# Performance work log

Hardware: AMD Instinct MI355X
Metric: run time of the kernel (lower is better)

Reference implementation:

```python
import jax, jax.numpy as jnp
import numpy as np
from math import tan, cos, sin

FOVX, FOVY = 1.2, 0.9
ZNEAR, ZFAR = 0.1, 100.0
HEIGHT, WIDTH = 1080, 1920
RELAX = 1.3
N = 2_000_000


def get_projection_matrix():
    # faithful to Camera.get_projection_matrix (symmetric frustum)
    right = ZNEAR * tan(0.5 * FOVX)
    top = ZNEAR * tan(0.5 * FOVY)
    left, bottom = -right, -top
    return jnp.array([
        [2 * ZNEAR / (right - left), 0.0, (left + right) / (right - left), 0.0],
        [0.0, 2 * ZNEAR / (top - bottom), (top + bottom) / (top - bottom), 0.0],
        [0.0, 0.0, ZFAR / (ZFAR - ZNEAR), -ZFAR * ZNEAR / (ZFAR - ZNEAR)],
        [0.0, 0.0, 1.0, 0.0]], dtype=jnp.float32)


def setup_inputs() -> dict:
    key = jax.random.key(0)
    k1, k2, k3 = jax.random.split(key, 3)
    # Gaussians spread in front of the camera: xy ~ N(0,3^2), z in [0.5, 20]
    xy = 3.0 * jax.random.normal(k1, (N, 2), dtype=jnp.float32)
    z = jax.random.uniform(k2, (N, 1), dtype=jnp.float32, minval=0.5, maxval=20.0)
    pos3d = jnp.concatenate([xy, z], axis=1)
    # PSD covariances: A A^T with small scale
    A = 0.1 * jax.random.normal(k3, (N, 3, 3), dtype=jnp.float32)
    cov3d = jnp.einsum('nij,nkj->nik', A, A)
    # rigid world->camera pose: small rotation about y + translation
    th = 0.1
    R = np.array([[cos(th), 0, sin(th)], [0, 1, 0], [-sin(th), 0, cos(th)]], dtype=np.float32)
    t = np.array([0.1, -0.2, 0.3], dtype=np.float32)
    W2C = np.eye(4, dtype=np.float32)
    W2C[:3, :3] = R
    W2C[:3, 3] = t
    world2model = jnp.asarray(W2C)
    return {"pos3d": pos3d, "cov3d": cov3d, "world2model": world2model}


def reference(pos3d, cov3d, world2model):
    n = pos3d.shape[0]
    P = get_projection_matrix()
    R = world2model[:3, :3]
    t = world2model[:3, 3]
    # view transform: ppos @ view_matrix[:3,:3] + view_matrix[3,:3] with view = W2C^T
    p_model = pos3d @ R.T + t                                  # [N,3]
    p_h = jnp.concatenate([p_model, jnp.ones((n, 1), pos3d.dtype)], axis=1)
    p_clip = p_h @ P.T                                         # [N,4]
    p_ndc = p_clip[:, :3] / (p_clip[:, 3:4] + 1e-6)            # [N,3]
    # cull mask (intended semantics of the buggy torch expression)
    mask = ((p_ndc[:, 2] >= 0.2)
            & (p_ndc[:, 0] >= -RELAX) & (p_ndc[:, 0] <= RELAX)
            & (p_ndc[:, 1] >= -RELAX) & (p_ndc[:, 1] <= RELAX))
    # ndc -> pixel coords, depth kept in 3rd slot
    px = 0.5 * (p_ndc[:, 0] + 1.0) * WIDTH
    py = (1.0 - 0.5 * (p_ndc[:, 1] + 1.0)) * HEIGHT
    pos2d = jnp.stack([px, py, p_ndc[:, 2]], axis=1)           # [N,3]
    pos2d = jnp.where(mask[:, None], pos2d, 0.0)
    # covariance projection: J @ W @ cov @ W^T @ J^T, W = R^T, J from world pos (as in source)
    Wm = R.T
    inv_z = 1.0 / pos3d[:, 2]
    zcol = jnp.zeros_like(inv_z)
    J = jnp.stack([
        jnp.stack([inv_z, zcol, -pos3d[:, 0] * inv_z], axis=1),
        jnp.stack([zcol, inv_z, -pos3d[:, 1] * inv_z], axis=1)], axis=1)  # [N,2,3]
    M = jnp.einsum('nij,jk->nik', J, Wm)                       # [N,2,3]
    cov2d = jnp.einsum('nij,njk,nlk->nil', M, cov3d, M)        # [N,2,2]
    cov2d = jnp.where(mask[:, None, None], cov2d, 0.0)
    return pos2d, cov2d, mask
```

## Files before the change

### kernel.cpp

```cpp
#include <hip/hip_runtime.h>
#include <math.h>


__global__ __launch_bounds__(256) void camera_kernel(
    const float* __restrict__ pos3d,
    const float* __restrict__ cov3d,
    const float* __restrict__ w2m,
    float* __restrict__ pos2d,
    float* __restrict__ cov2d,
    float* __restrict__ maskf,
    int n, float fx, float fy, float pA, float pB)
{
    int i = blockIdx.x * blockDim.x + threadIdx.x;
    if (i >= n) return;

    const float R00 = w2m[0], R01 = w2m[1], R02 = w2m[2],  t0 = w2m[3];
    const float R10 = w2m[4], R11 = w2m[5], R12 = w2m[6],  t1 = w2m[7];
    const float R20 = w2m[8], R21 = w2m[9], R22 = w2m[10], t2 = w2m[11];

    const float x = pos3d[3*i + 0];
    const float y = pos3d[3*i + 1];
    const float z = pos3d[3*i + 2];

    const float pmx = R00*x + R01*y + R02*z + t0;
    const float pmy = R10*x + R11*y + R12*z + t1;
    const float pmz = R20*x + R21*y + R22*z + t2;

    const float invw = 1.0f / (pmz + 1e-6f);
    const float ndcx = fx * pmx * invw;
    const float ndcy = fy * pmy * invw;
    const float ndcz = (pA * pmz + pB) * invw;

    const bool m = (ndcz >= 0.2f) && (ndcx >= -1.3f) && (ndcx <= 1.3f)
                                  && (ndcy >= -1.3f) && (ndcy <= 1.3f);

    const float px = 0.5f * (ndcx + 1.0f) * 1920.0f;
    const float py = (1.0f - 0.5f * (ndcy + 1.0f)) * 1080.0f;

    pos2d[3*i + 0] = m ? px   : 0.0f;
    pos2d[3*i + 1] = m ? py   : 0.0f;
    pos2d[3*i + 2] = m ? ndcz : 0.0f;

    const float invz = 1.0f / z;
    const float M00 = invz * (R00 - x * R02);
    const float M01 = invz * (R10 - x * R12);
    const float M02 = invz * (R20 - x * R22);
    const float M10 = invz * (R01 - y * R02);
    const float M11 = invz * (R11 - y * R12);
    const float M12 = invz * (R21 - y * R22);

    const float c00 = cov3d[9*i + 0], c01 = cov3d[9*i + 1], c02 = cov3d[9*i + 2];
    const float c10 = cov3d[9*i + 3], c11 = cov3d[9*i + 4], c12 = cov3d[9*i + 5];
    const float c20 = cov3d[9*i + 6], c21 = cov3d[9*i + 7], c22 = cov3d[9*i + 8];

    const float T00 = M00*c00 + M01*c10 + M02*c20;
    const float T01 = M00*c01 + M01*c11 + M02*c21;
    const float T02 = M00*c02 + M01*c12 + M02*c22;
    const float T10 = M10*c00 + M11*c10 + M12*c20;
    const float T11 = M10*c01 + M11*c11 + M12*c21;
    const float T12 = M10*c02 + M11*c12 + M12*c22;

    float4 cv;
    cv.x = m ? (T00*M00 + T01*M01 + T02*M02) : 0.0f;
    cv.y = m ? (T00*M10 + T01*M11 + T02*M12) : 0.0f;
    cv.z = m ? (T10*M00 + T11*M01 + T12*M02) : 0.0f;
    cv.w = m ? (T10*M10 + T11*M11 + T12*M12) : 0.0f;
    reinterpret_cast<float4*>(cov2d)[i] = cv;

    maskf[i] = m ? 1.0f : 0.0f;
}

extern "C" void kernel_launch(void* const* d_in, const int* in_sizes, int n_in,
                              void* d_out, int out_size, void* d_ws, size_t ws_size,
                              hipStream_t stream) {
    const float* pos3d = (const float*)d_in[0];
    const float* cov3d = (const float*)d_in[1];
    const float* w2m   = (const float*)d_in[2];

    const int n = in_sizes[0] / 3;

    float* out   = (float*)d_out;
    float* pos2d = out;
    float* cov2d = out + 3*(size_t)n;
    float* maskf = out + 7*(size_t)n;

    const double right = 0.1 * tan(0.5 * 1.2);
    const double top   = 0.1 * tan(0.5 * 0.9);
    const float fx = (float)(2.0 * 0.1 / (2.0 * right));
    const float fy = (float)(2.0 * 0.1 / (2.0 * top));
    const float pA = (float)(100.0 / (100.0 - 0.1));
    const float pB = (float)(-100.0 * 0.1 / (100.0 - 0.1));

    const int block = 256;
    const int grid = (n + block - 1) / block;
    camera_kernel<<<grid, block, 0, stream>>>(pos3d, cov3d, w2m,
                                              pos2d, cov2d, maskf,
                                              n, fx, fy, pA, pB);
}
```

Baseline: 28.31 us.

## Stage AoS position and covariance loads/stores through shared memory with float4 coalescing

Each block cooperatively copies its 256 points' pos3d and cov3d records into LDS using float4 vector loads, then threads read their own records from LDS. Projected positions are written back into LDS and stored to global memory as coalesced float4 chunks. This targets the strided 12- and 36-byte per-thread accesses of the array-of-structs layout. It adds three block barriers and LDS traffic, and raises shared memory use per block, which may lower occupancy.

```diff
diff --git a/kernel.cpp b/kernel.cpp
--- a/kernel.cpp
+++ b/kernel.cpp
@@ -2,7 +2,9 @@
 #include <math.h>
 
 
-__global__ __launch_bounds__(256) void camera_kernel(
+#define PTS 256
+
+__global__ __launch_bounds__(256) void camera_lds(
     const float* __restrict__ pos3d,
     const float* __restrict__ cov3d,
     const float* __restrict__ w2m,
@@ -11,63 +13,103 @@
     float* __restrict__ maskf,
     int n, float fx, float fy, float pA, float pB)
 {
-    int i = blockIdx.x * blockDim.x + threadIdx.x;
-    if (i >= n) return;
+    __shared__ float4 sp4[PTS * 3 / 4];
+    __shared__ float4 sc4[PTS * 9 / 4];
+    float* spf = reinterpret_cast<float*>(sp4);
+    float* scf = reinterpret_cast<float*>(sc4);
+
+    const int tid = threadIdx.x;
+    const int b0  = blockIdx.x * PTS;
+    const int pc  = min(PTS, n - b0);
+
+    {
+        const int npos = 3 * pc;
+        const float* gp = pos3d + (size_t)3 * b0;
+        const int nf4 = npos >> 2;
+        const float4* gp4 = reinterpret_cast<const float4*>(gp);
+        for (int q = tid; q < nf4; q += 256) sp4[q] = gp4[q];
+        for (int q = (nf4 << 2) + tid; q < npos; q += 256) spf[q] = gp[q];
+
+        const int ncov = 9 * pc;
+        const float* gc = cov3d + (size_t)9 * b0;
+        const int cf4 = ncov >> 2;
+        const float4* gc4 = reinterpret_cast<const float4*>(gc);
+        for (int q = tid; q < cf4; q += 256) sc4[q] = gc4[q];
+        for (int q = (cf4 << 2) + tid; q < ncov; q += 256) scf[q] = gc[q];
+    }
+    __syncthreads();
+
+    const bool act = (tid < pc);
+    const int i = b0 + tid;
+
+    float x = 0.0f, y = 0.0f, z = 1.0f;
+    float c00=0,c01=0,c02=0,c10=0,c11=0,c12=0,c20=0,c21=0,c22=0;
+    if (act) {
+        x = spf[3*tid+0]; y = spf[3*tid+1]; z = spf[3*tid+2];
+        c00 = scf[9*tid+0]; c01 = scf[9*tid+1]; c02 = scf[9*tid+2];
+        c10 = scf[9*tid+3]; c11 = scf[9*tid+4]; c12 = scf[9*tid+5];
+        c20 = scf[9*tid+6]; c21 = scf[9*tid+7]; c22 = scf[9*tid+8];
+    }
+    __syncthreads();
 
     const float R00 = w2m[0], R01 = w2m[1], R02 = w2m[2],  t0 = w2m[3];
     const float R10 = w2m[4], R11 = w2m[5], R12 = w2m[6],  t1 = w2m[7];
     const float R20 = w2m[8], R21 = w2m[9], R22 = w2m[10], t2 = w2m[11];
 
-    const float x = pos3d[3*i + 0];
-    const float y = pos3d[3*i + 1];
-    const float z = pos3d[3*i + 2];
+    if (act) {
+        const float pmx = R00*x + R01*y + R02*z + t0;
+        const float pmy = R10*x + R11*y + R12*z + t1;
+        const float pmz = R20*x + R21*y + R22*z + t2;
 
-    const float pmx = R00*x + R01*y + R02*z + t0;
-    const float pmy = R10*x + R11*y + R12*z + t1;
-    const float pmz = R20*x + R21*y + R22*z + t2;
+        const float invw = 1.0f / (pmz + 1e-6f);
+        const float ndcx = fx * pmx * invw;
+        const float ndcy = fy * pmy * invw;
+        const float ndcz = (pA * pmz + pB) * invw;
 
-    const float invw = 1.0f / (pmz + 1e-6f);
-    const float ndcx = fx * pmx * invw;
-    const float ndcy = fy * pmy * invw;
-    const float ndcz = (pA * pmz + pB) * invw;
+        const bool m = (ndcz >= 0.2f) && (ndcx >= -1.3f) && (ndcx <= 1.3f)
+                                      && (ndcy >= -1.3f) && (ndcy <= 1.3f);
 
-    const bool m = (ndcz >= 0.2f) && (ndcx >= -1.3f) && (ndcx <= 1.3f)
-                                  && (ndcy >= -1.3f) && (ndcy <= 1.3f);
+        const float px = 0.5f * (ndcx + 1.0f) * 1920.0f;
+        const float py = (1.0f - 0.5f * (ndcy + 1.0f)) * 1080.0f;
 
-    const float px = 0.5f * (ndcx + 1.0f) * 1920.0f;
-    const float py = (1.0f - 0.5f * (ndcy + 1.0f)) * 1080.0f;
+        spf[3*tid+0] = m ? px   : 0.0f;
+        spf[3*tid+1] = m ? py   : 0.0f;
+        spf[3*tid+2] = m ? ndcz : 0.0f;
 
-    pos2d[3*i + 0] = m ? px   : 0.0f;
-    pos2d[3*i + 1] = m ? py   : 0.0f;
-    pos2d[3*i + 2] = m ? ndcz : 0.0f;
+        const float invz = 1.0f / z;
+        const float M00 = invz * (R00 - x * R02);
+        const float M01 = invz * (R10 - x * R12);
+        const float M02 = invz * (R20 - x * R22);
+        const float M10 = invz * (R01 - y * R02);
+        const float M11 = invz * (R11 - y * R12);
+        const float M12 = invz * (R21 - y * R22);
 
-    const float invz = 1.0f / z;
-    const float M00 = invz * (R00 - x * R02);
-    const float M01 = invz * (R10 - x * R12);
-    const float M02 = invz * (R20 - x * R22);
-    const float M10 = invz * (R01 - y * R02);
-    const float M11 = invz * (R11 - y * R12);
-    const float M12 = invz * (R21 - y * R22);
+        const float T00 = M00*c00 + M01*c10 + M02*c20;
+        const float T01 = M00*c01 + M01*c11 + M02*c21;
+        const float T02 = M00*c02 + M01*c12 + M02*c22;
+        const float T10 = M10*c00 + M11*c10 + M12*c20;
+        const float T11 = M10*c01 + M11*c11 + M12*c21;
+        const float T12 = M10*c02 + M11*c12 + M12*c22;
 
-    const float c00 = cov3d[9*i + 0], c01 = cov3d[9*i + 1], c02 = cov3d[9*i + 2];
-    const float c10 = cov3d[9*i + 3], c11 = cov3d[9*i + 4], c12 = cov3d[9*i + 5];
-    const float c20 = cov3d[9*i + 6], c21 = cov3d[9*i + 7], c22 = cov3d[9*i + 8];
+        float4 cv;
+        cv.x = m ? (T00*M00 + T01*M01 + T02*M02) : 0.0f;
+        cv.y = m ? (T00*M10 + T01*M11 + T02*M12) : 0.0f;
+        cv.z = m ? (T10*M00 + T11*M01 + T12*M02) : 0.0f;
+        cv.w = m ? (T10*M10 + T11*M11 + T12*M12) : 0.0f;
+        reinterpret_cast<float4*>(cov2d)[i] = cv;
 
-    const float T00 = M00*c00 + M01*c10 + M02*c20;
-    const float T01 = M00*c01 + M01*c11 + M02*c21;
-    const float T02 = M00*c02 + M01*c12 + M02*c22;
-    const float T10 = M10*c00 + M11*c10 + M12*c20;
-    const float T11 = M10*c01 + M11*c11 + M12*c21;
-    const float T12 = M10*c02 + M11*c12 + M12*c22;
+        maskf[i] = m ? 1.0f : 0.0f;
+    }
+    __syncthreads();
 
-    float4 cv;
-    cv.x = m ? (T00*M00 + T01*M01 + T02*M02) : 0.0f;
-    cv.y = m ? (T00*M10 + T01*M11 + T02*M12) : 0.0f;
-    cv.z = m ? (T10*M00 + T11*M01 + T12*M02) : 0.0f;
-    cv.w = m ? (T10*M10 + T11*M11 + T12*M12) : 0.0f;
-    reinterpret_cast<float4*>(cov2d)[i] = cv;
-
-    maskf[i] = m ? 1.0f : 0.0f;
+    {
+        const int npos = 3 * pc;
+        float* go = pos2d + (size_t)3 * b0;
+        const int nf4 = npos >> 2;
+        float4* go4 = reinterpret_cast<float4*>(go);
+        for (int q = tid; q < nf4; q += 256) go4[q] = sp4[q];
+        for (int q = (nf4 << 2) + tid; q < npos; q += 256) go[q] = spf[q];
+    }
 }
 
 extern "C" void kernel_launch(void* const* d_in, const int* in_sizes, int n_in,
@@ -91,9 +133,8 @@
     const float pA = (float)(100.0 / (100.0 - 0.1));
     const float pB = (float)(-100.0 * 0.1 / (100.0 - 0.1));
 
-    const int block = 256;
-    const int grid = (n + block - 1) / block;
-    camera_kernel<<<grid, block, 0, stream>>>(pos3d, cov3d, w2m,
-                                              pos2d, cov2d, maskf,
-                                              n, fx, fy, pA, pB);
+    const int grid = (n + PTS - 1) / PTS;
+    camera_lds<<<grid, 256, 0, stream>>>(pos3d, cov3d, w2m,
+                                         pos2d, cov2d, maskf,
+                                         n, fx, fy, pA, pB);
 }
```

Result: slower. 29.68 us (+4.8%).

## Batch four elements per thread with loads issued before compute

Applied to the files above, without the earlier changes.

Replaces the one-thread-per-element launch with a fixed 2048-block grid where each thread processes four strided elements. It first loads all positions and covariances into registers, then computes and stores, to increase outstanding memory requests per thread. This raises register pressure and assumes n fits within grid*ITER elements, since there is no outer loop.

```diff
diff --git a/kernel.cpp b/kernel.cpp
--- a/kernel.cpp
+++ b/kernel.cpp
@@ -2,7 +2,10 @@
 #include <math.h>
 
 
-__global__ __launch_bounds__(256) void camera_kernel(
+#define BLK  256
+#define ITER 4
+
+__global__ __launch_bounds__(256) void camera_gs(
     const float* __restrict__ pos3d,
     const float* __restrict__ cov3d,
     const float* __restrict__ w2m,
@@ -11,63 +14,89 @@
     float* __restrict__ maskf,
     int n, float fx, float fy, float pA, float pB)
 {
-    int i = blockIdx.x * blockDim.x + threadIdx.x;
-    if (i >= n) return;
+    const int t0 = blockIdx.x * BLK + threadIdx.x;
+    const int G  = gridDim.x * BLK;
 
-    const float R00 = w2m[0], R01 = w2m[1], R02 = w2m[2],  t0 = w2m[3];
-    const float R10 = w2m[4], R11 = w2m[5], R12 = w2m[6],  t1 = w2m[7];
-    const float R20 = w2m[8], R21 = w2m[9], R22 = w2m[10], t2 = w2m[11];
+    const float R00 = w2m[0], R01 = w2m[1], R02 = w2m[2],  tr0 = w2m[3];
+    const float R10 = w2m[4], R11 = w2m[5], R12 = w2m[6],  tr1 = w2m[7];
+    const float R20 = w2m[8], R21 = w2m[9], R22 = w2m[10], tr2 = w2m[11];
 
-    const float x = pos3d[3*i + 0];
-    const float y = pos3d[3*i + 1];
-    const float z = pos3d[3*i + 2];
+    float p[ITER * 3];
+    float C[ITER * 9];
+    bool  vld[ITER];
 
-    const float pmx = R00*x + R01*y + R02*z + t0;
-    const float pmy = R10*x + R11*y + R12*z + t1;
-    const float pmz = R20*x + R21*y + R22*z + t2;
+    #pragma unroll
+    for (int k = 0; k < ITER; ++k) {
+        const int i = t0 + k * G;
+        const bool v = (i < n);
+        vld[k] = v;
+        if (v) {
+            p[3*k+0] = pos3d[3*(size_t)i + 0];
+            p[3*k+1] = pos3d[3*(size_t)i + 1];
+            p[3*k+2] = pos3d[3*(size_t)i + 2];
+            #pragma unroll
+            for (int q = 0; q < 9; ++q) C[9*k+q] = cov3d[9*(size_t)i + q];
+        } else {
+            p[3*k+0] = p[3*k+1] = 0.0f; p[3*k+2] = 1.0f;
+            #pragma unroll
+            for (int q = 0; q < 9; ++q) C[9*k+q] = 0.0f;
+        }
+    }
 
-    const float invw = 1.0f / (pmz + 1e-6f);
-    const float ndcx = fx * pmx * invw;
-    const float ndcy = fy * pmy * invw;
-    const float ndcz = (pA * pmz + pB) * invw;
+    #pragma unroll
+    for (int k = 0; k < ITER; ++k) {
+        if (!vld[k]) continue;
+        const int i = t0 + k * G;
 
-    const bool m = (ndcz >= 0.2f) && (ndcx >= -1.3f) && (ndcx <= 1.3f)
-                                  && (ndcy >= -1.3f) && (ndcy <= 1.3f);
+        const float x = p[3*k+0], y = p[3*k+1], z = p[3*k+2];
 
-    const float px = 0.5f * (ndcx + 1.0f) * 1920.0f;
-    const float py = (1.0f - 0.5f * (ndcy + 1.0f)) * 1080.0f;
+        const float pmx = R00*x + R01*y + R02*z + tr0;
+        const float pmy = R10*x + R11*y + R12*z + tr1;
+        const float pmz = R20*x + R21*y + R22*z + tr2;
 
-    pos2d[3*i + 0] = m ? px   : 0.0f;
-    pos2d[3*i + 1] = m ? py   : 0.0f;
-    pos2d[3*i + 2] = m ? ndcz : 0.0f;
+        const float invw = 1.0f / (pmz + 1e-6f);
+        const float ndcx = fx * pmx * invw;
+        const float ndcy = fy * pmy * invw;
+        const float ndcz = (pA * pmz + pB) * invw;
 
-    const float invz = 1.0f / z;
-    const float M00 = invz * (R00 - x * R02);
-    const float M01 = invz * (R10 - x * R12);
-    const float M02 = invz * (R20 - x * R22);
-    const float M10 = invz * (R01 - y * R02);
-    const float M11 = invz * (R11 - y * R12);
-    const float M12 = invz * (R21 - y * R22);
+        const bool m = (ndcz >= 0.2f) && (ndcx >= -1.3f) && (ndcx <= 1.3f)
+                                      && (ndcy >= -1.3f) && (ndcy <= 1.3f);
 
-    const float c00 = cov3d[9*i + 0], c01 = cov3d[9*i + 1], c02 = cov3d[9*i + 2];
-    const float c10 = cov3d[9*i + 3], c11 = cov3d[9*i + 4], c12 = cov3d[9*i + 5];
-    const float c20 = cov3d[9*i + 6], c21 = cov3d[9*i + 7], c22 = cov3d[9*i + 8];
+        const float px = 0.5f * (ndcx + 1.0f) * 1920.0f;
+        const float py = (1.0f - 0.5f * (ndcy + 1.0f)) * 1080.0f;
 
-    const float T00 = M00*c00 + M01*c10 + M02*c20;
-    const float T01 = M00*c01 + M01*c11 + M02*c21;
-    const float T02 = M00*c02 + M01*c12 + M02*c22;
-    const float T10 = M10*c00 + M11*c10 + M12*c20;
-    const float T11 = M10*c01 + M11*c11 + M12*c21;
-    const float T12 = M10*c02 + M11*c12 + M12*c22;
+        pos2d[3*(size_t)i + 0] = m ? px   : 0.0f;
+        pos2d[3*(size_t)i + 1] = m ? py   : 0.0f;
+        pos2d[3*(size_t)i + 2] = m ? ndcz : 0.0f;
 
-    float4 cv;
-    cv.x = m ? (T00*M00 + T01*M01 + T02*M02) : 0.0f;
-    cv.y = m ? (T00*M10 + T01*M11 + T02*M12) : 0.0f;
-    cv.z = m ? (T10*M00 + T11*M01 + T12*M02) : 0.0f;
-    cv.w = m ? (T10*M10 + T11*M11 + T12*M12) : 0.0f;
-    reinterpret_cast<float4*>(cov2d)[i] = cv;
+        const float invz = 1.0f / z;
+        const float M00 = invz * (R00 - x * R02);
+        const float M01 = invz * (R10 - x * R12);
+        const float M02 = invz * (R20 - x * R22);
+        const float M10 = invz * (R01 - y * R02);
+        const float M11 = invz * (R11 - y * R12);
+        const float M12 = invz * (R21 - y * R22);
 
-    maskf[i] = m ? 1.0f : 0.0f;
+        const float c00 = C[9*k+0], c01 = C[9*k+1], c02 = C[9*k+2];
+        const float c10 = C[9*k+3], c11 = C[9*k+4], c12 = C[9*k+5];
+        const float c20 = C[9*k+6], c21 = C[9*k+7], c22 = C[9*k+8];
+
+        const float T00 = M00*c00 + M01*c10 + M02*c20;
+        const float T01 = M00*c01 + M01*c11 + M02*c21;
+        const float T02 = M00*c02 + M01*c12 + M02*c22;
+        const float T10 = M10*c00 + M11*c10 + M12*c20;
+        const float T11 = M10*c01 + M11*c11 + M12*c21;
+        const float T12 = M10*c02 + M11*c12 + M12*c22;
+
+        float4 cv;
+        cv.x = m ? (T00*M00 + T01*M01 + T02*M02) : 0.0f;
+        cv.y = m ? (T00*M10 + T01*M11 + T02*M12) : 0.0f;
+        cv.z = m ? (T10*M00 + T11*M01 + T12*M02) : 0.0f;
+        cv.w = m ? (T10*M10 + T11*M11 + T12*M12) : 0.0f;
+        reinterpret_cast<float4*>(cov2d)[i] = cv;
+
+        maskf[i] = m ? 1.0f : 0.0f;
+    }
 }
 
 extern "C" void kernel_launch(void* const* d_in, const int* in_sizes, int n_in,
@@ -91,9 +120,8 @@
     const float pA = (float)(100.0 / (100.0 - 0.1));
     const float pB = (float)(-100.0 * 0.1 / (100.0 - 0.1));
 
-    const int block = 256;
-    const int grid = (n + block - 1) / block;
-    camera_kernel<<<grid, block, 0, stream>>>(pos3d, cov3d, w2m,
-                                              pos2d, cov2d, maskf,
-                                              n, fx, fy, pA, pB);
+    const int grid = 2048;
+    camera_gs<<<grid, BLK, 0, stream>>>(pos3d, cov3d, w2m,
+                                        pos2d, cov2d, maskf,
+                                        n, fx, fy, pA, pB);
 }
```

New measurement: 29.52 us. +4.3%, slower.
